# Kernel tuning notes

Measured on AMD Instinct MI355X. Metric: run time of the kernel, lower is better.

Reference implementation:

```python
import jax, jax.numpy as jnp
import numpy as np

F_DIM = 2
L_LEVELS = 16
N_MIN, N_MAX = 16, 2048
_B = np.exp((np.log(N_MAX) - np.log(N_MIN)) / (L_LEVELS - 1))
NL = np.array([int(np.floor(N_MIN * _B ** l)) for l in range(L_LEVELS)], dtype=np.float32)
T_SIZE = 2 ** 19
AABB = 3.0
N_PTS = 262144
N_FREQ_DIR = 4  # direction PE frequencies -> 3 + 3*2*4 = 27 dims (matches color_MLP input 16+27)
PIS = np.array([1, 2654435761, 805459861], dtype=np.uint32)
# 8 cube-corner offsets; order matches the torch vertex enumeration
OFFS = np.array([[0,0,0],[1,0,0],[0,1,0],[1,1,0],[0,0,1],[1,0,1],[0,1,1],[1,1,1]], dtype=np.float32)


def _hash_encode(xn, tables):
    # xn: [N,3] normalized positions in ~[0,1); tables: [L,T,F]
    Ns = jnp.asarray(NL)                                   # [L]
    scaled = xn[None, :, :] * Ns[:, None, None]            # [L,N,3]
    fl = jnp.floor(scaled)
    loc = scaled - fl                                      # [L,N,3] trilinear weights
    offs_i = jnp.asarray(OFFS, jnp.int32)                  # [8,3]
    verts = fl.astype(jnp.int32)[:, :, None, :] + offs_i[None, None]   # [L,N,8,3]
    v = verts.astype(jnp.uint32)
    pis = jnp.asarray(PIS)
    h = ((v[..., 0] * pis[0]) ^ (v[..., 1] * pis[1]) ^ (v[..., 2] * pis[2])) % jnp.uint32(T_SIZE)
    idx = h.astype(jnp.int32)                              # [L,N,8]
    corner = jax.vmap(lambda t, i: t[i])(tables, idx)      # [L,N,8,F] hashed gather
    offs = jnp.asarray(OFFS)                               # [8,3]
    w = jnp.prod(offs[None, None] * loc[:, :, None, :] + (1.0 - offs[None, None]) * (1.0 - loc[:, :, None, :]), axis=-1)  # [L,N,8]
    feats = jnp.einsum('lnc,lncf->lnf', w, corner)         # [L,N,F]
    N = xn.shape[0]
    return feats.transpose(1, 0, 2).reshape(N, L_LEVELS * F_DIM)  # [N, L*F]


def _pos_enc_dir(d):
    outs = [d]
    for j in range(N_FREQ_DIR):
        outs.append(jnp.sin((2.0 ** j) * d))
        outs.append(jnp.cos((2.0 ** j) * d))
    return jnp.concatenate(outs, axis=1)                   # [N,27]


def setup_inputs() -> dict:
    key = jax.random.key(0)
    ks = jax.random.split(key, 12)
    x = jax.random.normal(ks[0], (N_PTS, 3), jnp.float32)
    d = jax.random.normal(ks[1], (N_PTS, 3), jnp.float32)
    tables = (jax.random.uniform(ks[2], (L_LEVELS, T_SIZE, F_DIM), jnp.float32) * 2.0 - 1.0) * 1e-4
    def lin(k, fi, fo):
        return jax.random.normal(k, (fi, fo), jnp.float32) * (1.0 / np.sqrt(fi))
    return {
        'x': x, 'd': d, 'tables': tables,
        'dW1': lin(ks[3], 32, 64), 'db1': jnp.zeros((64,), jnp.float32),
        'dW2': lin(ks[4], 64, 16), 'db2': jnp.zeros((16,), jnp.float32),
        'cW1': lin(ks[5], 43, 64), 'cb1': jnp.zeros((64,), jnp.float32),
        'cW2': lin(ks[6], 64, 64), 'cb2': jnp.zeros((64,), jnp.float32),
        'cW3': lin(ks[7], 64, 3), 'cb3': jnp.zeros((3,), jnp.float32),
    }


def reference(x, d, tables, dW1, db1, dW2, db2, cW1, cb1, cW2, cb2, cW3, cb3):
    xn = x / AABB
    mask = (jnp.abs(xn[:, 0]) < 0.5) & (jnp.abs(xn[:, 1]) < 0.5) & (jnp.abs(xn[:, 2]) < 0.5)
    xn = xn + 0.5
    feats = _hash_encode(xn, tables)                        # [N,32]
    h = jnp.maximum(feats @ dW1 + db1, 0.0) @ dW2 + db2     # [N,16]
    d_enc = _pos_enc_dir(d)                                 # [N,27]
    ch = jnp.concatenate([h, d_enc], axis=1)                # [N,43]
    ch = jnp.maximum(ch @ cW1 + cb1, 0.0)
    ch = jnp.maximum(ch @ cW2 + cb2, 0.0)
    rgb = jax.nn.sigmoid(ch @ cW3 + cb3)                    # [N,3]
    sigma = jnp.where(mask, h[:, 0], jnp.float32(-100000.0))
    rgb = jnp.where(mask[:, None], rgb, 0.0)
    return rgb, jnp.exp(sigma)
```

## Files before the change

kernel.cpp:

```cpp
#include <hip/hip_runtime.h>

#define NPTS 262144
#define HP1 2654435761u
#define HP2 805459861u
#define TMASK 0x7FFFFu

typedef __attribute__((ext_vector_type(8))) short short8;
typedef __attribute__((ext_vector_type(4))) float f32x4;
typedef unsigned short ushort_t;
typedef unsigned int uint_t;

#define MFMA(a, b, c) __builtin_amdgcn_mfma_f32_16x16x32_bf16((a), (b), (c), 0, 0, 0)

__device__ __forceinline__ ushort_t f2bf(float f) {
    uint_t u = __float_as_uint(f);
    return (ushort_t)((u + 0x7FFFu + ((u >> 16) & 1u)) >> 16);
}
__device__ __forceinline__ float sigmoidf_fast(float v) {
    return 1.0f / (1.0f + __expf(-v));
}

#define OFF_DW1 0
#define OFF_DW2 2048
#define OFF_CW1 3072
#define OFF_CW2 7168
#define OFF_CW3 11264
#define WF_TOTAL 12288

extern "C" __global__ void ngp_prep(
    const float* __restrict__ dW1, const float* __restrict__ dW2,
    const float* __restrict__ cW1, const float* __restrict__ cW2,
    const float* __restrict__ cW3, ushort_t* __restrict__ wf)
{
    const int e = blockIdx.x * 256 + (int)threadIdx.x;
    if (e >= WF_TOTAL) return;
    const float* W; int base, NT, KR, NR;
    if (e < OFF_DW2)      { W = dW1; base = OFF_DW1; NT = 4; KR = 32; NR = 64; }
    else if (e < OFF_CW1) { W = dW2; base = OFF_DW2; NT = 1; KR = 64; NR = 16; }
    else if (e < OFF_CW2) { W = cW1; base = OFF_CW1; NT = 4; KR = 43; NR = 64; }
    else if (e < OFF_CW3) { W = cW2; base = OFF_CW2; NT = 4; KR = 64; NR = 64; }
    else                  { W = cW3; base = OFF_CW3; NT = 1; KR = 64; NR = 3;  }
    const int r = e - base;
    const int frag = r >> 9;
    const int lane = (r >> 3) & 63;
    const int j = r & 7;
    const int kc = frag / NT, nt = frag % NT;
    const int k = kc * 32 + ((lane >> 4) << 3) + j;
    const int n = nt * 16 + (lane & 15);
    const float v = (k < KR && n < NR) ? W[k * NR + n] : 0.0f;
    wf[e] = f2bf(v);
}

extern "C" __global__ void __launch_bounds__(256) ngp_encode(
    const float* __restrict__ xin, const float* __restrict__ tbl,
    uint_t* __restrict__ feats)
{
    const int l  = blockIdx.x >> 10;
    const int pt = ((blockIdx.x & 1023) << 8) + (int)threadIdx.x;

    const float x0 = xin[3 * pt + 0];
    const float x1 = xin[3 * pt + 1];
    const float x2 = xin[3 * pt + 2];
    const float xn0 = x0 / 3.0f, xn1 = x1 / 3.0f, xn2 = x2 / 3.0f;
    const bool mask = (fabsf(xn0) < 0.5f) & (fabsf(xn1) < 0.5f) & (fabsf(xn2) < 0.5f);
    if (!mask) return;

    static const float NLs[16] = {16.f, 22.f, 30.f, 42.f, 58.f, 80.f, 111.f, 153.f,
                                  212.f, 294.f, 406.f, 561.f, 776.f, 1072.f, 1482.f, 2048.f};
    const float nl = NLs[l];

    const float s0 = (xn0 + 0.5f) * nl;
    const float s1 = (xn1 + 0.5f) * nl;
    const float s2 = (xn2 + 0.5f) * nl;
    const float f0 = floorf(s0), f1 = floorf(s1), f2 = floorf(s2);
    const float l0 = s0 - f0, l1 = s1 - f1, l2 = s2 - f2;

    const unsigned va0 = (unsigned)(int)f0;
    const unsigned vb0 = va0 + 1u;
    const unsigned va1 = (unsigned)(int)f1 * HP1;
    const unsigned vb1 = va1 + HP1;
    const unsigned va2 = (unsigned)(int)f2 * HP2;
    const unsigned vb2 = va2 + HP2;

    const float2* tp = (const float2*)tbl + (size_t)l * 524288u;

    const unsigned i000 = (va0 ^ va1 ^ va2) & TMASK;
    const unsigned i100 = (vb0 ^ va1 ^ va2) & TMASK;
    const unsigned i010 = (va0 ^ vb1 ^ va2) & TMASK;
    const unsigned i110 = (vb0 ^ vb1 ^ va2) & TMASK;
    const unsigned i001 = (va0 ^ va1 ^ vb2) & TMASK;
    const unsigned i101 = (vb0 ^ va1 ^ vb2) & TMASK;
    const unsigned i011 = (va0 ^ vb1 ^ vb2) & TMASK;
    const unsigned i111 = (vb0 ^ vb1 ^ vb2) & TMASK;

    const float2 c000 = tp[i000];
    const float2 c100 = tp[i100];
    const float2 c010 = tp[i010];
    const float2 c110 = tp[i110];
    const float2 c001 = tp[i001];
    const float2 c101 = tp[i101];
    const float2 c011 = tp[i011];
    const float2 c111 = tp[i111];

    const float m0 = 1.0f - l0, m1 = 1.0f - l1, m2 = 1.0f - l2;
    float a = 0.0f, b = 0.0f, w;
    w = m0 * m1 * m2; a = fmaf(w, c000.x, a); b = fmaf(w, c000.y, b);
    w = l0 * m1 * m2; a = fmaf(w, c100.x, a); b = fmaf(w, c100.y, b);
    w = m0 * l1 * m2; a = fmaf(w, c010.x, a); b = fmaf(w, c010.y, b);
    w = l0 * l1 * m2; a = fmaf(w, c110.x, a); b = fmaf(w, c110.y, b);
    w = m0 * m1 * l2; a = fmaf(w, c001.x, a); b = fmaf(w, c001.y, b);
    w = l0 * m1 * l2; a = fmaf(w, c101.x, a); b = fmaf(w, c101.y, b);
    w = m0 * l1 * l2; a = fmaf(w, c011.x, a); b = fmaf(w, c011.y, b);
    w = l0 * l1 * l2; a = fmaf(w, c111.x, a); b = fmaf(w, c111.y, b);

    feats[(size_t)l * NPTS + pt] = (uint_t)f2bf(a) | ((uint_t)f2bf(b) << 16);
}

extern "C" __global__ void __launch_bounds__(256) ngp_mlp(
    const float* __restrict__ xin, const float* __restrict__ din,
    const uint_t* __restrict__ featsbf, const ushort_t* __restrict__ wf,
    const float* __restrict__ db1, const float* __restrict__ db2,
    const float* __restrict__ cb1, const float* __restrict__ cb2,
    const float* __restrict__ cb3,
    float* __restrict__ out)
{
    __shared__ short act[4][4096];
    __shared__ float mk[4][64];

    const int w    = (int)threadIdx.x >> 6;
    const int lane = (int)threadIdx.x & 63;
    const int lrow = lane & 15;
    const int lq   = lane >> 4;
    const int ptb  = blockIdx.x * 256 + w * 64;
    const int p    = ptb + lane;
    char* Ab = (char*)&act[w][0];

#define LDSA(mt, kc) (*reinterpret_cast<const short8*>(Ab + ((((mt) * 16 + lrow) * 128 + (kc) * 64 + lq * 16) ^ ((lrow & 7) << 4))))
#define LOADB(off)   (*reinterpret_cast<const short8*>(wf + (off) + lane * 8))
#define STB16(row, col, val) *reinterpret_cast<ushort_t*>(Ab + ((((row) * 128 + (col) * 2)) ^ (((row) & 7) << 4))) = (val)

    const float x0 = xin[3 * p + 0];
    const float x1 = xin[3 * p + 1];
    const float x2 = xin[3 * p + 2];
    const bool msk = (fabsf(x0) < 1.5f) & (fabsf(x1) < 1.5f) & (fabsf(x2) < 1.5f);
    mk[w][lane] = msk ? 1.0f : 0.0f;

    uint_t u[16];
    #pragma unroll
    for (int l = 0; l < 16; ++l) u[l] = featsbf[(size_t)l * NPTS + p];
    #pragma unroll
    for (int c = 0; c < 4; ++c) {
        short8 v;
        #pragma unroll
        for (int q = 0; q < 4; ++q) {
            v[2 * q + 0] = (short)(u[4 * c + q] & 0xFFFFu);
            v[2 * q + 1] = (short)(u[4 * c + q] >> 16);
        }
        const int byte = (lane * 128 + 16 * c) ^ ((lane & 7) << 4);
        *reinterpret_cast<short8*>(Ab + byte) = v;
    }
    const float d0v = din[3 * p + 0];
    const float d1v = din[3 * p + 1];
    const float d2v = din[3 * p + 2];

    __syncthreads();

    f32x4 acc[4][4];
    #pragma unroll
    for (int nt = 0; nt < 4; ++nt) {
        const float b = db1[nt * 16 + lrow];
        #pragma unroll
        for (int mt = 0; mt < 4; ++mt) acc[mt][nt] = (f32x4){b, b, b, b};
    }
    {
        short8 a0 = LDSA(0, 0), a1 = LDSA(1, 0), a2 = LDSA(2, 0), a3 = LDSA(3, 0);
        #pragma unroll
        for (int nt = 0; nt < 4; ++nt) {
            const short8 B = LOADB(OFF_DW1 + nt * 512);
            acc[0][nt] = MFMA(a0, B, acc[0][nt]);
            acc[1][nt] = MFMA(a1, B, acc[1][nt]);
            acc[2][nt] = MFMA(a2, B, acc[2][nt]);
            acc[3][nt] = MFMA(a3, B, acc[3][nt]);
        }
    }
    __syncthreads();
    #pragma unroll
    for (int mt = 0; mt < 4; ++mt)
        #pragma unroll
        for (int nt = 0; nt < 4; ++nt)
            #pragma unroll
            for (int r = 0; r < 4; ++r) {
                const int row = mt * 16 + lq * 4 + r;
                STB16(row, nt * 16 + lrow, f2bf(fmaxf(acc[mt][nt][r], 0.0f)));
            }
    __syncthreads();

    f32x4 hD[4];
    {
        const float b = db2[lrow];
        #pragma unroll
        for (int mt = 0; mt < 4; ++mt) hD[mt] = (f32x4){b, b, b, b};
        #pragma unroll
        for (int kc = 0; kc < 2; ++kc) {
            const short8 B = LOADB(OFF_DW2 + kc * 512);
            #pragma unroll
            for (int mt = 0; mt < 4; ++mt) hD[mt] = MFMA(LDSA(mt, kc), B, hD[mt]);
        }
    }
    __syncthreads();

    if (lrow == 0) {
        #pragma unroll
        for (int mt = 0; mt < 4; ++mt)
            #pragma unroll
            for (int r = 0; r < 4; ++r) {
                const int row = mt * 16 + lq * 4 + r;
                const float mm = mk[w][row];
                out[3 * NPTS + ptb + row] = (mm != 0.0f) ? __expf(hD[mt][r]) : 0.0f;
            }
    }
    #pragma unroll
    for (int mt = 0; mt < 4; ++mt)
        #pragma unroll
        for (int r = 0; r < 4; ++r) {
            const int row = mt * 16 + lq * 4 + r;
            STB16(row, lrow, f2bf(hD[mt][r]));
        }
    {
        ushort_t t[48];
        t[0] = f2bf(d0v); t[1] = f2bf(d1v); t[2] = f2bf(d2v);
        #pragma unroll
        for (int j = 0; j < 4; ++j) {
            const float s = (float)(1 << j);
            t[3 + 6 * j + 0] = f2bf(__sinf(s * d0v));
            t[3 + 6 * j + 1] = f2bf(__sinf(s * d1v));
            t[3 + 6 * j + 2] = f2bf(__sinf(s * d2v));
            t[3 + 6 * j + 3] = f2bf(__cosf(s * d0v));
            t[3 + 6 * j + 4] = f2bf(__cosf(s * d1v));
            t[3 + 6 * j + 5] = f2bf(__cosf(s * d2v));
        }
        #pragma unroll
        for (int i = 27; i < 48; ++i) t[i] = 0;
        #pragma unroll
        for (int c = 0; c < 6; ++c) {
            short8 v;
            #pragma unroll
            for (int j = 0; j < 8; ++j) v[j] = (short)t[8 * c + j];
            const int byte = (lane * 128 + 32 + 16 * c) ^ ((lane & 7) << 4);
            *reinterpret_cast<short8*>(Ab + byte) = v;
        }
    }
    __syncthreads();

    #pragma unroll
    for (int nt = 0; nt < 4; ++nt) {
        const float b = cb1[nt * 16 + lrow];
        #pragma unroll
        for (int mt = 0; mt < 4; ++mt) acc[mt][nt] = (f32x4){b, b, b, b};
    }
    #pragma unroll
    for (int kc = 0; kc < 2; ++kc) {
        short8 a0 = LDSA(0, kc), a1 = LDSA(1, kc), a2 = LDSA(2, kc), a3 = LDSA(3, kc);
        #pragma unroll
        for (int nt = 0; nt < 4; ++nt) {
            const short8 B = LOADB(OFF_CW1 + (kc * 4 + nt) * 512);
            acc[0][nt] = MFMA(a0, B, acc[0][nt]);
            acc[1][nt] = MFMA(a1, B, acc[1][nt]);
            acc[2][nt] = MFMA(a2, B, acc[2][nt]);
            acc[3][nt] = MFMA(a3, B, acc[3][nt]);
        }
    }
    __syncthreads();
    #pragma unroll
    for (int mt = 0; mt < 4; ++mt)
        #pragma unroll
        for (int nt = 0; nt < 4; ++nt)
            #pragma unroll
            for (int r = 0; r < 4; ++r) {
                const int row = mt * 16 + lq * 4 + r;
                STB16(row, nt * 16 + lrow, f2bf(fmaxf(acc[mt][nt][r], 0.0f)));
            }
    __syncthreads();

    #pragma unroll
    for (int nt = 0; nt < 4; ++nt) {
        const float b = cb2[nt * 16 + lrow];
        #pragma unroll
        for (int mt = 0; mt < 4; ++mt) acc[mt][nt] = (f32x4){b, b, b, b};
    }
    #pragma unroll
    for (int kc = 0; kc < 2; ++kc) {
        short8 a0 = LDSA(0, kc), a1 = LDSA(1, kc), a2 = LDSA(2, kc), a3 = LDSA(3, kc);
        #pragma unroll
        for (int nt = 0; nt < 4; ++nt) {
            const short8 B = LOADB(OFF_CW2 + (kc * 4 + nt) * 512);
            acc[0][nt] = MFMA(a0, B, acc[0][nt]);
            acc[1][nt] = MFMA(a1, B, acc[1][nt]);
            acc[2][nt] = MFMA(a2, B, acc[2][nt]);
            acc[3][nt] = MFMA(a3, B, acc[3][nt]);
        }
    }
    __syncthreads();
    #pragma unroll
    for (int mt = 0; mt < 4; ++mt)
        #pragma unroll
        for (int nt = 0; nt < 4; ++nt)
            #pragma unroll
            for (int r = 0; r < 4; ++r) {
                const int row = mt * 16 + lq * 4 + r;
                STB16(row, nt * 16 + lrow, f2bf(fmaxf(acc[mt][nt][r], 0.0f)));
            }
    __syncthreads();

    f32x4 rD[4];
    {
        const float b = (lrow < 3) ? cb3[lrow] : 0.0f;
        #pragma unroll
        for (int mt = 0; mt < 4; ++mt) rD[mt] = (f32x4){b, b, b, b};
        #pragma unroll
        for (int kc = 0; kc < 2; ++kc) {
            const short8 B = LOADB(OFF_CW3 + kc * 512);
            #pragma unroll
            for (int mt = 0; mt < 4; ++mt) rD[mt] = MFMA(LDSA(mt, kc), B, rD[mt]);
        }
    }
    if (lrow < 3) {
        #pragma unroll
        for (int mt = 0; mt < 4; ++mt)
            #pragma unroll
            for (int r = 0; r < 4; ++r) {
                const int row = mt * 16 + lq * 4 + r;
                const float mm = mk[w][row];
                out[3 * (ptb + row) + lrow] = (mm != 0.0f) ? sigmoidf_fast(rD[mt][r]) : 0.0f;
            }
    }
#undef LDSA
#undef LOADB
#undef STB16
}

extern "C" void kernel_launch(void* const* d_in, const int* in_sizes, int n_in,
                              void* d_out, int out_size, void* d_ws, size_t ws_size,
                              hipStream_t stream) {
    const float* x    = (const float*)d_in[0];
    const float* d    = (const float*)d_in[1];
    const float* tbl  = (const float*)d_in[2];
    const float* dW1  = (const float*)d_in[3];
    const float* db1  = (const float*)d_in[4];
    const float* dW2  = (const float*)d_in[5];
    const float* db2  = (const float*)d_in[6];
    const float* cW1  = (const float*)d_in[7];
    const float* cb1  = (const float*)d_in[8];
    const float* cW2  = (const float*)d_in[9];
    const float* cb2  = (const float*)d_in[10];
    const float* cW3  = (const float*)d_in[11];
    const float* cb3  = (const float*)d_in[12];

    uint_t* feats = (uint_t*)d_ws;
    ushort_t* wfr = (ushort_t*)((char*)d_ws + 16u * 1024u * 1024u);

    ngp_prep<<<48, 256, 0, stream>>>(dW1, dW2, cW1, cW2, cW3, wfr);
    ngp_encode<<<16 * 1024, 256, 0, stream>>>(x, tbl, feats);
    ngp_mlp<<<NPTS / 256, 256, 0, stream>>>(
        x, d, feats, wfr, db1, db2, cb1, cb2, cb3, (float*)d_out);
}
```

Measured before the change: 108.1 us.

## Convert hash tables to bf16 before gather and interleave levels across blocks

Adds a pass that converts the full fp32 hash table (16 levels x 512K x 2 floats, 64 MB) to packed bf16 pairs in workspace, so each corner gather in the encoder reads 4 bytes instead of 8. The encoder block mapping also changes so that consecutive blocks process 8 different levels for the same points, which may improve L2 locality of point reads and spread table traffic. In exchange, every call pays a full streaming read of 64 MB and a write of 32 MB, and table values lose precision to bf16.

```diff
diff --git a/kernel.cpp b/kernel.cpp
--- a/kernel.cpp
+++ b/kernel.cpp
@@ -16,9 +16,15 @@
     uint_t u = __float_as_uint(f);
     return (ushort_t)((u + 0x7FFFu + ((u >> 16) & 1u)) >> 16);
 }
+__device__ __forceinline__ float bf2f(ushort_t b) {
+    return __uint_as_float(((uint_t)b) << 16);
+}
 __device__ __forceinline__ float sigmoidf_fast(float v) {
     return 1.0f / (1.0f + __expf(-v));
 }
+
+#define WS_TBL_OFF  (16u * 1024u * 1024u)
+#define WS_WF_OFF   (48u * 1024u * 1024u)
 
 #define OFF_DW1 0
 #define OFF_DW2 2048
@@ -26,6 +32,17 @@
 #define OFF_CW2 7168
 #define OFF_CW3 11264
 #define WF_TOTAL 12288
+
+extern "C" __global__ void __launch_bounds__(256) ngp_tblconv(
+    const float4* __restrict__ tbl, uint2* __restrict__ tblbf)
+{
+    const int g = blockIdx.x * 256 + (int)threadIdx.x;
+    const float4 v = tbl[g];
+    uint2 o;
+    o.x = (uint_t)f2bf(v.x) | ((uint_t)f2bf(v.y) << 16);
+    o.y = (uint_t)f2bf(v.z) | ((uint_t)f2bf(v.w) << 16);
+    tblbf[g] = o;
+}
 
 extern "C" __global__ void ngp_prep(
     const float* __restrict__ dW1, const float* __restrict__ dW2,
@@ -52,11 +69,13 @@
 }
 
 extern "C" __global__ void __launch_bounds__(256) ngp_encode(
-    const float* __restrict__ xin, const float* __restrict__ tbl,
+    const float* __restrict__ xin, const uint_t* __restrict__ tblbf,
     uint_t* __restrict__ feats)
 {
-    const int l  = blockIdx.x >> 10;
-    const int pt = ((blockIdx.x & 1023) << 8) + (int)threadIdx.x;
+    const int b = blockIdx.x;
+    const int j = b >> 3;
+    const int l = (b & 7) + ((j & 1) << 3);
+    const int pt = ((j >> 1) << 8) + (int)threadIdx.x;
 
     const float x0 = xin[3 * pt + 0];
     const float x1 = xin[3 * pt + 1];
@@ -82,7 +101,7 @@
     const unsigned va2 = (unsigned)(int)f2 * HP2;
     const unsigned vb2 = va2 + HP2;
 
-    const float2* tp = (const float2*)tbl + (size_t)l * 524288u;
+    const uint_t* tp = tblbf + (size_t)l * 524288u;
 
     const unsigned i000 = (va0 ^ va1 ^ va2) & TMASK;
     const unsigned i100 = (vb0 ^ va1 ^ va2) & TMASK;
@@ -93,27 +112,27 @@
     const unsigned i011 = (va0 ^ vb1 ^ vb2) & TMASK;
     const unsigned i111 = (vb0 ^ vb1 ^ vb2) & TMASK;
 
-    const float2 c000 = tp[i000];
-    const float2 c100 = tp[i100];
-    const float2 c010 = tp[i010];
-    const float2 c110 = tp[i110];
-    const float2 c001 = tp[i001];
-    const float2 c101 = tp[i101];
-    const float2 c011 = tp[i011];
-    const float2 c111 = tp[i111];
+    const uint_t c000 = tp[i000];
+    const uint_t c100 = tp[i100];
+    const uint_t c010 = tp[i010];
+    const uint_t c110 = tp[i110];
+    const uint_t c001 = tp[i001];
+    const uint_t c101 = tp[i101];
+    const uint_t c011 = tp[i011];
+    const uint_t c111 = tp[i111];
 
     const float m0 = 1.0f - l0, m1 = 1.0f - l1, m2 = 1.0f - l2;
-    float a = 0.0f, b = 0.0f, w;
-    w = m0 * m1 * m2; a = fmaf(w, c000.x, a); b = fmaf(w, c000.y, b);
-    w = l0 * m1 * m2; a = fmaf(w, c100.x, a); b = fmaf(w, c100.y, b);
-    w = m0 * l1 * m2; a = fmaf(w, c010.x, a); b = fmaf(w, c010.y, b);
-    w = l0 * l1 * m2; a = fmaf(w, c110.x, a); b = fmaf(w, c110.y, b);
-    w = m0 * m1 * l2; a = fmaf(w, c001.x, a); b = fmaf(w, c001.y, b);
-    w = l0 * m1 * l2; a = fmaf(w, c101.x, a); b = fmaf(w, c101.y, b);
-    w = m0 * l1 * l2; a = fmaf(w, c011.x, a); b = fmaf(w, c011.y, b);
-    w = l0 * l1 * l2; a = fmaf(w, c111.x, a); b = fmaf(w, c111.y, b);
-
-    feats[(size_t)l * NPTS + pt] = (uint_t)f2bf(a) | ((uint_t)f2bf(b) << 16);
+    float a = 0.0f, bb = 0.0f, w;
+    w = m0 * m1 * m2; a = fmaf(w, bf2f((ushort_t)c000), a); bb = fmaf(w, bf2f((ushort_t)(c000 >> 16)), bb);
+    w = l0 * m1 * m2; a = fmaf(w, bf2f((ushort_t)c100), a); bb = fmaf(w, bf2f((ushort_t)(c100 >> 16)), bb);
+    w = m0 * l1 * m2; a = fmaf(w, bf2f((ushort_t)c010), a); bb = fmaf(w, bf2f((ushort_t)(c010 >> 16)), bb);
+    w = l0 * l1 * m2; a = fmaf(w, bf2f((ushort_t)c110), a); bb = fmaf(w, bf2f((ushort_t)(c110 >> 16)), bb);
+    w = m0 * m1 * l2; a = fmaf(w, bf2f((ushort_t)c001), a); bb = fmaf(w, bf2f((ushort_t)(c001 >> 16)), bb);
+    w = l0 * m1 * l2; a = fmaf(w, bf2f((ushort_t)c101), a); bb = fmaf(w, bf2f((ushort_t)(c101 >> 16)), bb);
+    w = m0 * l1 * l2; a = fmaf(w, bf2f((ushort_t)c011), a); bb = fmaf(w, bf2f((ushort_t)(c011 >> 16)), bb);
+    w = l0 * l1 * l2; a = fmaf(w, bf2f((ushort_t)c111), a); bb = fmaf(w, bf2f((ushort_t)(c111 >> 16)), bb);
+
+    feats[(size_t)l * NPTS + pt] = (uint_t)f2bf(a) | ((uint_t)f2bf(bb) << 16);
 }
 
 extern "C" __global__ void __launch_bounds__(256) ngp_mlp(
@@ -356,11 +375,13 @@
     const float* cW3  = (const float*)d_in[11];
     const float* cb3  = (const float*)d_in[12];
 
-    uint_t* feats = (uint_t*)d_ws;
-    ushort_t* wfr = (ushort_t*)((char*)d_ws + 16u * 1024u * 1024u);
-
+    uint_t* feats   = (uint_t*)d_ws;
+    uint_t* tblbf   = (uint_t*)((char*)d_ws + WS_TBL_OFF);
+    ushort_t* wfr   = (ushort_t*)((char*)d_ws + WS_WF_OFF);
+
+    ngp_tblconv<<<16384, 256, 0, stream>>>((const float4*)tbl, (uint2*)tblbf);
     ngp_prep<<<48, 256, 0, stream>>>(dW1, dW2, cW1, cW2, cW3, wfr);
-    ngp_encode<<<16 * 1024, 256, 0, stream>>>(x, tbl, feats);
+    ngp_encode<<<16 * 1024, 256, 0, stream>>>(x, tblbf, feats);
     ngp_mlp<<<NPTS / 256, 256, 0, stream>>>(
         x, d, feats, wfr, db1, db2, cb1, cb2, cb3, (float*)d_out);
 }
```

New measurement: 132.6 us. +22.7%, slower.

## Fuse hash-grid encoding into the MLP kernel, dropping the feature buffer

Applied to the files above, without the earlier changes.

Moves the per-level hash-grid trilinear gather into the MLP kernel, computing all 16 levels per point in registers instead of a separate encode kernel writing bf16 features to workspace. This removes the 16 MB feature round trip through global memory and one kernel launch. In exchange, each thread gathers across all level tables, which loses the per-level cache locality of the old layout, and register pressure rises in an already large kernel.

```diff
diff --git a/kernel.cpp b/kernel.cpp
--- a/kernel.cpp
+++ b/kernel.cpp
@@ -51,74 +51,9 @@
     wf[e] = f2bf(v);
 }
 
-extern "C" __global__ void __launch_bounds__(256) ngp_encode(
-    const float* __restrict__ xin, const float* __restrict__ tbl,
-    uint_t* __restrict__ feats)
-{
-    const int l  = blockIdx.x >> 10;
-    const int pt = ((blockIdx.x & 1023) << 8) + (int)threadIdx.x;
-
-    const float x0 = xin[3 * pt + 0];
-    const float x1 = xin[3 * pt + 1];
-    const float x2 = xin[3 * pt + 2];
-    const float xn0 = x0 / 3.0f, xn1 = x1 / 3.0f, xn2 = x2 / 3.0f;
-    const bool mask = (fabsf(xn0) < 0.5f) & (fabsf(xn1) < 0.5f) & (fabsf(xn2) < 0.5f);
-    if (!mask) return;
-
-    static const float NLs[16] = {16.f, 22.f, 30.f, 42.f, 58.f, 80.f, 111.f, 153.f,
-                                  212.f, 294.f, 406.f, 561.f, 776.f, 1072.f, 1482.f, 2048.f};
-    const float nl = NLs[l];
-
-    const float s0 = (xn0 + 0.5f) * nl;
-    const float s1 = (xn1 + 0.5f) * nl;
-    const float s2 = (xn2 + 0.5f) * nl;
-    const float f0 = floorf(s0), f1 = floorf(s1), f2 = floorf(s2);
-    const float l0 = s0 - f0, l1 = s1 - f1, l2 = s2 - f2;
-
-    const unsigned va0 = (unsigned)(int)f0;
-    const unsigned vb0 = va0 + 1u;
-    const unsigned va1 = (unsigned)(int)f1 * HP1;
-    const unsigned vb1 = va1 + HP1;
-    const unsigned va2 = (unsigned)(int)f2 * HP2;
-    const unsigned vb2 = va2 + HP2;
-
-    const float2* tp = (const float2*)tbl + (size_t)l * 524288u;
-
-    const unsigned i000 = (va0 ^ va1 ^ va2) & TMASK;
-    const unsigned i100 = (vb0 ^ va1 ^ va2) & TMASK;
-    const unsigned i010 = (va0 ^ vb1 ^ va2) & TMASK;
-    const unsigned i110 = (vb0 ^ vb1 ^ va2) & TMASK;
-    const unsigned i001 = (va0 ^ va1 ^ vb2) & TMASK;
-    const unsigned i101 = (vb0 ^ va1 ^ vb2) & TMASK;
-    const unsigned i011 = (va0 ^ vb1 ^ vb2) & TMASK;
-    const unsigned i111 = (vb0 ^ vb1 ^ vb2) & TMASK;
-
-    const float2 c000 = tp[i000];
-    const float2 c100 = tp[i100];
-    const float2 c010 = tp[i010];
-    const float2 c110 = tp[i110];
-    const float2 c001 = tp[i001];
-    const float2 c101 = tp[i101];
-    const float2 c011 = tp[i011];
-    const float2 c111 = tp[i111];
-
-    const float m0 = 1.0f - l0, m1 = 1.0f - l1, m2 = 1.0f - l2;
-    float a = 0.0f, b = 0.0f, w;
-    w = m0 * m1 * m2; a = fmaf(w, c000.x, a); b = fmaf(w, c000.y, b);
-    w = l0 * m1 * m2; a = fmaf(w, c100.x, a); b = fmaf(w, c100.y, b);
-    w = m0 * l1 * m2; a = fmaf(w, c010.x, a); b = fmaf(w, c010.y, b);
-    w = l0 * l1 * m2; a = fmaf(w, c110.x, a); b = fmaf(w, c110.y, b);
-    w = m0 * m1 * l2; a = fmaf(w, c001.x, a); b = fmaf(w, c001.y, b);
-    w = l0 * m1 * l2; a = fmaf(w, c101.x, a); b = fmaf(w, c101.y, b);
-    w = m0 * l1 * l2; a = fmaf(w, c011.x, a); b = fmaf(w, c011.y, b);
-    w = l0 * l1 * l2; a = fmaf(w, c111.x, a); b = fmaf(w, c111.y, b);
-
-    feats[(size_t)l * NPTS + pt] = (uint_t)f2bf(a) | ((uint_t)f2bf(b) << 16);
-}
-
-extern "C" __global__ void __launch_bounds__(256) ngp_mlp(
+extern "C" __global__ void __launch_bounds__(256) ngp_fused(
     const float* __restrict__ xin, const float* __restrict__ din,
-    const uint_t* __restrict__ featsbf, const ushort_t* __restrict__ wf,
+    const float* __restrict__ tbl, const ushort_t* __restrict__ wf,
     const float* __restrict__ db1, const float* __restrict__ db2,
     const float* __restrict__ cb1, const float* __restrict__ cb2,
     const float* __restrict__ cb3,
@@ -142,12 +77,66 @@
     const float x0 = xin[3 * p + 0];
     const float x1 = xin[3 * p + 1];
     const float x2 = xin[3 * p + 2];
-    const bool msk = (fabsf(x0) < 1.5f) & (fabsf(x1) < 1.5f) & (fabsf(x2) < 1.5f);
+    const float xn0 = x0 / 3.0f, xn1 = x1 / 3.0f, xn2 = x2 / 3.0f;
+    const bool msk = (fabsf(xn0) < 0.5f) & (fabsf(xn1) < 0.5f) & (fabsf(xn2) < 0.5f);
     mk[w][lane] = msk ? 1.0f : 0.0f;
 
     uint_t u[16];
     #pragma unroll
-    for (int l = 0; l < 16; ++l) u[l] = featsbf[(size_t)l * NPTS + p];
+    for (int l = 0; l < 16; ++l) u[l] = 0u;
+    if (msk) {
+        static const float NLs[16] = {16.f, 22.f, 30.f, 42.f, 58.f, 80.f, 111.f, 153.f,
+                                      212.f, 294.f, 406.f, 561.f, 776.f, 1072.f, 1482.f, 2048.f};
+        const float q0 = xn0 + 0.5f, q1 = xn1 + 0.5f, q2 = xn2 + 0.5f;
+        #pragma unroll
+        for (int l = 0; l < 16; ++l) {
+            const float nl = NLs[l];
+            const float s0 = q0 * nl, s1 = q1 * nl, s2 = q2 * nl;
+            const float f0 = floorf(s0), f1 = floorf(s1), f2 = floorf(s2);
+            const float l0 = s0 - f0, l1 = s1 - f1, l2 = s2 - f2;
+
+            const unsigned va0 = (unsigned)(int)f0;
+            const unsigned vb0 = va0 + 1u;
+            const unsigned va1 = (unsigned)(int)f1 * HP1;
+            const unsigned vb1 = va1 + HP1;
+            const unsigned va2 = (unsigned)(int)f2 * HP2;
+            const unsigned vb2 = va2 + HP2;
+
+            const float2* tp = (const float2*)tbl + ((size_t)l << 19);
+
+            const unsigned i000 = (va0 ^ va1 ^ va2) & TMASK;
+            const unsigned i100 = (vb0 ^ va1 ^ va2) & TMASK;
+            const unsigned i010 = (va0 ^ vb1 ^ va2) & TMASK;
+            const unsigned i110 = (vb0 ^ vb1 ^ va2) & TMASK;
+            const unsigned i001 = (va0 ^ va1 ^ vb2) & TMASK;
+            const unsigned i101 = (vb0 ^ va1 ^ vb2) & TMASK;
+            const unsigned i011 = (va0 ^ vb1 ^ vb2) & TMASK;
+            const unsigned i111 = (vb0 ^ vb1 ^ vb2) & TMASK;
+
+            const float2 c000 = tp[i000];
+            const float2 c100 = tp[i100];
+            const float2 c010 = tp[i010];
+            const float2 c110 = tp[i110];
+            const float2 c001 = tp[i001];
+            const float2 c101 = tp[i101];
+            const float2 c011 = tp[i011];
+            const float2 c111 = tp[i111];
+
+            const float m0 = 1.0f - l0, m1 = 1.0f - l1, m2 = 1.0f - l2;
+            float a = 0.0f, bb = 0.0f, ww;
+            ww = m0 * m1 * m2; a = fmaf(ww, c000.x, a); bb = fmaf(ww, c000.y, bb);
+            ww = l0 * m1 * m2; a = fmaf(ww, c100.x, a); bb = fmaf(ww, c100.y, bb);
+            ww = m0 * l1 * m2; a = fmaf(ww, c010.x, a); bb = fmaf(ww, c010.y, bb);
+            ww = l0 * l1 * m2; a = fmaf(ww, c110.x, a); bb = fmaf(ww, c110.y, bb);
+            ww = m0 * m1 * l2; a = fmaf(ww, c001.x, a); bb = fmaf(ww, c001.y, bb);
+            ww = l0 * m1 * l2; a = fmaf(ww, c101.x, a); bb = fmaf(ww, c101.y, bb);
+            ww = m0 * l1 * l2; a = fmaf(ww, c011.x, a); bb = fmaf(ww, c011.y, bb);
+            ww = l0 * l1 * l2; a = fmaf(ww, c111.x, a); bb = fmaf(ww, c111.y, bb);
+
+            u[l] = (uint_t)f2bf(a) | ((uint_t)f2bf(bb) << 16);
+        }
+    }
+
     #pragma unroll
     for (int c = 0; c < 4; ++c) {
         short8 v;
@@ -356,11 +345,9 @@
     const float* cW3  = (const float*)d_in[11];
     const float* cb3  = (const float*)d_in[12];
 
-    uint_t* feats = (uint_t*)d_ws;
-    ushort_t* wfr = (ushort_t*)((char*)d_ws + 16u * 1024u * 1024u);
+    ushort_t* wfr = (ushort_t*)d_ws;
 
     ngp_prep<<<48, 256, 0, stream>>>(dW1, dW2, cW1, cW2, cW3, wfr);
-    ngp_encode<<<16 * 1024, 256, 0, stream>>>(x, tbl, feats);
-    ngp_mlp<<<NPTS / 256, 256, 0, stream>>>(
-        x, d, feats, wfr, db1, db2, cb1, cb2, cb3, (float*)d_out);
-}
+    ngp_fused<<<NPTS / 256, 256, 0, stream>>>(
+        x, d, tbl, wfr, db1, db2, cb1, cb2, cb3, (float*)d_out);
+}
```

New measurement: 139.6 us. +29.2%, slower.

## Precompute dense corner-pair grids for coarse levels and pair-load hashed fine levels

Applied to the files above, without the earlier changes.

Adds a pre-pass that, for the five coarsest levels, expands the hash table into a dense grid. Each entry stores the x-adjacent corner pair as a float4, so encode needs four contiguous 16-byte loads instead of eight random 8-byte gathers. For the finer levels, when the x vertex is even the two x-neighbours hash to adjacent slots, so one aligned float4 load serves both. The cost is an extra kernel launch and about 5 MB of workspace traffic each call.

```diff
diff --git a/kernel.cpp b/kernel.cpp
--- a/kernel.cpp
+++ b/kernel.cpp
@@ -19,6 +19,16 @@
 __device__ __forceinline__ float sigmoidf_fast(float v) {
     return 1.0f / (1.0f + __expf(-v));
 }
+
+#define DOFF0 0
+#define DOFF1 4913
+#define DOFF2 17080
+#define DOFF3 46871
+#define DOFF4 126378
+#define DTOT  331757
+
+#define WS_DN_OFF (16u * 1024u * 1024u)
+#define WS_WF_OFF (22u * 1024u * 1024u)
 
 #define OFF_DW1 0
 #define OFF_DW2 2048
@@ -51,69 +61,122 @@
     wf[e] = f2bf(v);
 }
 
+extern "C" __global__ void ngp_dense(
+    const float* __restrict__ tbl, f32x4* __restrict__ dense)
+{
+    const int e = blockIdx.x * 256 + (int)threadIdx.x;
+    if (e >= DTOT) return;
+    int l, base, dim;
+    if (e < DOFF1)      { l = 0; base = DOFF0; dim = 17; }
+    else if (e < DOFF2) { l = 1; base = DOFF1; dim = 23; }
+    else if (e < DOFF3) { l = 2; base = DOFF2; dim = 31; }
+    else if (e < DOFF4) { l = 3; base = DOFF3; dim = 43; }
+    else                { l = 4; base = DOFF4; dim = 59; }
+    const int r = e - base;
+    const int v0 = r % dim;
+    const int t  = r / dim;
+    const int v1 = t % dim;
+    const int v2 = t / dim;
+    const float2* tp = (const float2*)tbl + ((size_t)l << 19);
+    const unsigned hy = (unsigned)v1 * HP1;
+    const unsigned hz = (unsigned)v2 * HP2;
+    const unsigned h0 = ((unsigned)v0 ^ hy ^ hz) & TMASK;
+    const unsigned h1 = (((unsigned)v0 + 1u) ^ hy ^ hz) & TMASK;
+    const float2 c0 = tp[h0];
+    const float2 c1 = tp[h1];
+    dense[e] = (f32x4){c0.x, c0.y, c1.x, c1.y};
+}
+
 extern "C" __global__ void __launch_bounds__(256) ngp_encode(
     const float* __restrict__ xin, const float* __restrict__ tbl,
-    uint_t* __restrict__ feats)
+    const f32x4* __restrict__ dense, uint_t* __restrict__ feats)
 {
-    const int l  = blockIdx.x >> 10;
-    const int pt = ((blockIdx.x & 1023) << 8) + (int)threadIdx.x;
+    const int b  = blockIdx.x;
+    const int l  = b >> 10;
+    const int pt = ((b & 1023) << 8) + (int)threadIdx.x;
+
+    static const float NLs[16] = {16.f, 22.f, 30.f, 42.f, 58.f, 80.f, 111.f, 153.f,
+                                  212.f, 294.f, 406.f, 561.f, 776.f, 1072.f, 1482.f, 2048.f};
+    static const int DDIM[5] = {17, 23, 31, 43, 59};
+    static const int DOFFS[5] = {DOFF0, DOFF1, DOFF2, DOFF3, DOFF4};
 
     const float x0 = xin[3 * pt + 0];
     const float x1 = xin[3 * pt + 1];
     const float x2 = xin[3 * pt + 2];
-    const float xn0 = x0 / 3.0f, xn1 = x1 / 3.0f, xn2 = x2 / 3.0f;
-    const bool mask = (fabsf(xn0) < 0.5f) & (fabsf(xn1) < 0.5f) & (fabsf(xn2) < 0.5f);
-    if (!mask) return;
-
-    static const float NLs[16] = {16.f, 22.f, 30.f, 42.f, 58.f, 80.f, 111.f, 153.f,
-                                  212.f, 294.f, 406.f, 561.f, 776.f, 1072.f, 1482.f, 2048.f};
+    const bool msk = (fabsf(x0) < 1.5f) & (fabsf(x1) < 1.5f) & (fabsf(x2) < 1.5f);
+    if (!msk) return;
+
     const float nl = NLs[l];
-
-    const float s0 = (xn0 + 0.5f) * nl;
-    const float s1 = (xn1 + 0.5f) * nl;
-    const float s2 = (xn2 + 0.5f) * nl;
+    const float s0 = (x0 / 3.0f + 0.5f) * nl;
+    const float s1 = (x1 / 3.0f + 0.5f) * nl;
+    const float s2 = (x2 / 3.0f + 0.5f) * nl;
     const float f0 = floorf(s0), f1 = floorf(s1), f2 = floorf(s2);
     const float l0 = s0 - f0, l1 = s1 - f1, l2 = s2 - f2;
-
-    const unsigned va0 = (unsigned)(int)f0;
-    const unsigned vb0 = va0 + 1u;
-    const unsigned va1 = (unsigned)(int)f1 * HP1;
-    const unsigned vb1 = va1 + HP1;
-    const unsigned va2 = (unsigned)(int)f2 * HP2;
-    const unsigned vb2 = va2 + HP2;
-
-    const float2* tp = (const float2*)tbl + (size_t)l * 524288u;
-
-    const unsigned i000 = (va0 ^ va1 ^ va2) & TMASK;
-    const unsigned i100 = (vb0 ^ va1 ^ va2) & TMASK;
-    const unsigned i010 = (va0 ^ vb1 ^ va2) & TMASK;
-    const unsigned i110 = (vb0 ^ vb1 ^ va2) & TMASK;
-    const unsigned i001 = (va0 ^ va1 ^ vb2) & TMASK;
-    const unsigned i101 = (vb0 ^ va1 ^ vb2) & TMASK;
-    const unsigned i011 = (va0 ^ vb1 ^ vb2) & TMASK;
-    const unsigned i111 = (vb0 ^ vb1 ^ vb2) & TMASK;
-
-    const float2 c000 = tp[i000];
-    const float2 c100 = tp[i100];
-    const float2 c010 = tp[i010];
-    const float2 c110 = tp[i110];
-    const float2 c001 = tp[i001];
-    const float2 c101 = tp[i101];
-    const float2 c011 = tp[i011];
-    const float2 c111 = tp[i111];
-
     const float m0 = 1.0f - l0, m1 = 1.0f - l1, m2 = 1.0f - l2;
-    float a = 0.0f, b = 0.0f, w;
-    w = m0 * m1 * m2; a = fmaf(w, c000.x, a); b = fmaf(w, c000.y, b);
-    w = l0 * m1 * m2; a = fmaf(w, c100.x, a); b = fmaf(w, c100.y, b);
-    w = m0 * l1 * m2; a = fmaf(w, c010.x, a); b = fmaf(w, c010.y, b);
-    w = l0 * l1 * m2; a = fmaf(w, c110.x, a); b = fmaf(w, c110.y, b);
-    w = m0 * m1 * l2; a = fmaf(w, c001.x, a); b = fmaf(w, c001.y, b);
-    w = l0 * m1 * l2; a = fmaf(w, c101.x, a); b = fmaf(w, c101.y, b);
-    w = m0 * l1 * l2; a = fmaf(w, c011.x, a); b = fmaf(w, c011.y, b);
-    w = l0 * l1 * l2; a = fmaf(w, c111.x, a); b = fmaf(w, c111.y, b);
-
-    feats[(size_t)l * NPTS + pt] = (uint_t)f2bf(a) | ((uint_t)f2bf(b) << 16);
+
+    float a = 0.0f, bb = 0.0f;
+
+    if (l < 5) {
+        const int dim = DDIM[l];
+        const f32x4* dp = dense + DOFFS[l];
+        const int idx = ((int)f2 * dim + (int)f1) * dim + (int)f0;
+        const f32x4 C00 = dp[idx];
+        const f32x4 C10 = dp[idx + dim];
+        const f32x4 C01 = dp[idx + dim * dim];
+        const f32x4 C11 = dp[idx + dim * dim + dim];
+        float w;
+        w = m1 * m2; a = fmaf(m0 * w, C00[0], a); bb = fmaf(m0 * w, C00[1], bb);
+                     a = fmaf(l0 * w, C00[2], a); bb = fmaf(l0 * w, C00[3], bb);
+        w = l1 * m2; a = fmaf(m0 * w, C10[0], a); bb = fmaf(m0 * w, C10[1], bb);
+                     a = fmaf(l0 * w, C10[2], a); bb = fmaf(l0 * w, C10[3], bb);
+        w = m1 * l2; a = fmaf(m0 * w, C01[0], a); bb = fmaf(m0 * w, C01[1], bb);
+                     a = fmaf(l0 * w, C01[2], a); bb = fmaf(l0 * w, C01[3], bb);
+        w = l1 * l2; a = fmaf(m0 * w, C11[0], a); bb = fmaf(m0 * w, C11[1], bb);
+                     a = fmaf(l0 * w, C11[2], a); bb = fmaf(l0 * w, C11[3], bb);
+    } else {
+        const float2* tp = (const float2*)tbl + ((size_t)l << 19);
+        const f32x4* tp4 = (const f32x4*)tp;
+        const unsigned v0 = (unsigned)(int)f0;
+        const unsigned hy0 = (unsigned)(int)f1 * HP1, hy1 = hy0 + HP1;
+        const unsigned hz0 = (unsigned)(int)f2 * HP2, hz1 = hz0 + HP2;
+        unsigned hyz[4];
+        hyz[0] = hy0 ^ hz0;
+        hyz[1] = hy1 ^ hz0;
+        hyz[2] = hy0 ^ hz1;
+        hyz[3] = hy1 ^ hz1;
+
+        float2 c[8];
+        if ((v0 & 1u) == 0u) {
+            #pragma unroll
+            for (int j = 0; j < 4; ++j) {
+                const unsigned hp = (v0 ^ hyz[j]) & TMASK;
+                const f32x4 blk = tp4[hp >> 1];
+                const float2 lo = {blk[0], blk[1]};
+                const float2 hi = {blk[2], blk[3]};
+                const bool sw = (hp & 1u) != 0u;
+                c[2 * j + 0] = sw ? hi : lo;
+                c[2 * j + 1] = sw ? lo : hi;
+            }
+        } else {
+            const unsigned vb0 = v0 + 1u;
+            #pragma unroll
+            for (int j = 0; j < 4; ++j) {
+                c[2 * j + 0] = tp[(v0  ^ hyz[j]) & TMASK];
+                c[2 * j + 1] = tp[(vb0 ^ hyz[j]) & TMASK];
+            }
+        }
+        float w;
+        w = m1 * m2; a = fmaf(m0 * w, c[0].x, a); bb = fmaf(m0 * w, c[0].y, bb);
+                     a = fmaf(l0 * w, c[1].x, a); bb = fmaf(l0 * w, c[1].y, bb);
+        w = l1 * m2; a = fmaf(m0 * w, c[2].x, a); bb = fmaf(m0 * w, c[2].y, bb);
+                     a = fmaf(l0 * w, c[3].x, a); bb = fmaf(l0 * w, c[3].y, bb);
+        w = m1 * l2; a = fmaf(m0 * w, c[4].x, a); bb = fmaf(m0 * w, c[4].y, bb);
+                     a = fmaf(l0 * w, c[5].x, a); bb = fmaf(l0 * w, c[5].y, bb);
+        w = l1 * l2; a = fmaf(m0 * w, c[6].x, a); bb = fmaf(m0 * w, c[6].y, bb);
+                     a = fmaf(l0 * w, c[7].x, a); bb = fmaf(l0 * w, c[7].y, bb);
+    }
+
+    feats[(size_t)l * NPTS + pt] = (uint_t)f2bf(a) | ((uint_t)f2bf(bb) << 16);
 }
 
 extern "C" __global__ void __launch_bounds__(256) ngp_mlp(
@@ -357,10 +420,12 @@
     const float* cb3  = (const float*)d_in[12];
 
     uint_t* feats = (uint_t*)d_ws;
-    ushort_t* wfr = (ushort_t*)((char*)d_ws + 16u * 1024u * 1024u);
+    f32x4* dense  = (f32x4*)((char*)d_ws + WS_DN_OFF);
+    ushort_t* wfr = (ushort_t*)((char*)d_ws + WS_WF_OFF);
 
     ngp_prep<<<48, 256, 0, stream>>>(dW1, dW2, cW1, cW2, cW3, wfr);
-    ngp_encode<<<16 * 1024, 256, 0, stream>>>(x, tbl, feats);
+    ngp_dense<<<(DTOT + 255) / 256, 256, 0, stream>>>(tbl, dense);
+    ngp_encode<<<16 * 1024, 256, 0, stream>>>(x, tbl, dense, feats);
     ngp_mlp<<<NPTS / 256, 256, 0, stream>>>(
         x, d, feats, wfr, db1, db2, cb1, cb2, cb3, (float*)d_out);
 }
```

New measurement: 112.5 us. 1.04x slower.
